# Optimization experiments

Measured on AMD Instinct MI355X. Metric: run time of the kernel, lower is better.

The kernel has to match this reference:

```python
import jax, jax.numpy as jnp
import numpy as np

NUM, B, C, H, W = 2, 8, 512, 32, 32


def setup_inputs() -> dict:
    key = jax.random.key(0)
    ks = jax.random.split(key, 6)
    s = 0.02  # weight init scale
    return {
        "feat_sources": jax.random.normal(ks[0], (NUM, B, C, H, W), jnp.float32),
        "feat_targets": jax.random.normal(ks[1], (NUM, B, C, H, W), jnp.float32),
        # 1x1 conv == per-pixel channel matmul: weight [num, C_out, C_in], bias [num, C]
        "Wq": jax.random.normal(ks[2], (NUM, C, C), jnp.float32) * s,
        "bq": jnp.zeros((NUM, C), jnp.float32),
        "Wk": jax.random.normal(ks[3], (NUM, C, C), jnp.float32) * s,
        "bk": jnp.zeros((NUM, C), jnp.float32),
        "Wv": jax.random.normal(ks[4], (NUM, C, C), jnp.float32) * s,
        "bv": jnp.zeros((NUM, C), jnp.float32),
    }


def reference(feat_sources, feat_targets, Wq, bq, Wk, bk, Wv, bv):
    num, Bt, Ct, Ht, Wt = feat_targets.shape
    HW = Ht * Wt
    tgt = feat_targets.reshape(num, Bt, Ct, HW)  # queries/values come from targets
    src = feat_sources.reshape(num, Bt, Ct, HW)  # keys come from sources

    # 1x1 conv projections (batched over the `num` heads of convs)
    Q = jnp.einsum('ioc,ibcn->ibno', Wq, tgt) + bq[:, None, None, :]   # (num, B, HW, C)
    K = jnp.einsum('joc,jbcn->jbon', Wk, src) + bk[:, None, :, None]   # (num, B, C, HW)
    V = jnp.einsum('ioc,ibcn->ibon', Wv, tgt) + bv[:, None, :, None]   # (num, B, C, HW)

    # energy[i, j] = bmm(pro_query_i, pro_key_j) over all target/source pairs
    energy = jnp.einsum('ibnc,jbcm->ijbnm', Q, K)                      # (num, num, B, HW, HW)

    # alpha: softmax over sources j of the scalar mean energy per (i, j)
    means = energy.mean(axis=(2, 3, 4))                                # (num, num)
    alphas = jax.nn.softmax(means, axis=1)

    # per-source softmax over keys, then summed across sources (torch.stack(...).sum(0))
    attn = jax.nn.softmax(energy, axis=-1).sum(axis=1)                 # (num, B, HW, HW)

    # out[b, c, n] = sum_m V[b, c, m] * attn[b, n, m]  (bmm(value, attention^T))
    out = jnp.einsum('ibcm,ibnm->ibcn', V, attn).reshape(num, Bt, Ct, Ht, Wt)
    return out, alphas
```

## Files before the change

kernel.cpp:

```cpp
#include <hip/hip_runtime.h>

#define NUMH 2
#define BATCH 8
#define CCH 512
#define HWN 1024

typedef unsigned short u16;
typedef unsigned int u32;
typedef _Float16 f16;
typedef __attribute__((ext_vector_type(8))) _Float16 f16x8;
typedef __attribute__((ext_vector_type(8))) short bf16x8;
typedef __attribute__((ext_vector_type(4))) float f32x4;

__device__ __forceinline__ u16 f2h(float x) {
    union { f16 h; u16 u; } cv;
    cv.h = (f16)x;
    return cv.u;
}
__device__ __forceinline__ u16 f2bf(float x) {
    u32 u = __float_as_uint(x);
    return (u16)((u + 0x7fffu + ((u >> 16) & 1u)) >> 16);
}

__device__ __forceinline__ float waveReduceSum(float v) {
#pragma unroll
    for (int off = 32; off > 0; off >>= 1) v += __shfl_xor(v, off);
    return v;
}

__device__ __forceinline__ void swz_decode(int& x, int& y, int& z) {
    const int gx = gridDim.x, gy = gridDim.y;
    const int nwg = gx * gy * gridDim.z;
    const int fid = blockIdx.x + gx * (blockIdx.y + gy * blockIdx.z);
    const int cpx = nwg >> 3;
    int swz = (fid & 7) * cpx + (fid >> 3);
    x = swz % gx; swz /= gx;
    y = swz % gy; z = swz / gy;
}

__global__ void zero_means_kernel(float* means) {
    if (threadIdx.x < 4) means[threadIdx.x] = 0.0f;
}
__global__ void zero_rs_kernel(float* rs, int n) {
    const int i = blockIdx.x * 256 + threadIdx.x;
    if (i < n) rs[i] = 0.0f;
}

__device__ __forceinline__ void stage_tile(const u16* __restrict__ src, int ld, int k0,
                                           u16* lds_arr, int w, int l) {
#pragma unroll
    for (int inst = 0; inst < 2; inst++) {
        const int p = w * 128 + inst * 64 + l;
        const int n = p >> 2;
        const int k4 = (p & 3) ^ ((n >> 1) & 3);
        const u16* g = src + n * ld + k0 + k4 * 8;
        u16* lp = lds_arr + (w * 128 + inst * 64) * 8;
        __builtin_amdgcn_global_load_lds(
            (const __attribute__((address_space(1))) u32*)g,
            (__attribute__((address_space(3))) u32*)lp, 16, 0, 0);
    }
}

template<bool BF>
__device__ __forceinline__ void mfma_block(const u16* sA, const u16* sB,
                                           int wr, int wc, int fr, int kq, f32x4 acc[4][4]) {
#define SLOT(row) (((row) * 4 + ((kq) ^ (((row) >> 1) & 3))) * 8)
    if constexpr (BF) {
        bf16x8 a[4], b[4];
#pragma unroll
        for (int mi = 0; mi < 4; mi++) a[mi] = *(const bf16x8*)(sA + SLOT(wr * 64 + mi * 16 + fr));
#pragma unroll
        for (int ni = 0; ni < 4; ni++) b[ni] = *(const bf16x8*)(sB + SLOT(wc * 64 + ni * 16 + fr));
#pragma unroll
        for (int mi = 0; mi < 4; mi++)
#pragma unroll
            for (int ni = 0; ni < 4; ni++)
                acc[mi][ni] = __builtin_amdgcn_mfma_f32_16x16x32_bf16(a[mi], b[ni], acc[mi][ni], 0, 0, 0);
    } else {
        f16x8 a[4], b[4];
#pragma unroll
        for (int mi = 0; mi < 4; mi++) a[mi] = *(const f16x8*)(sA + SLOT(wr * 64 + mi * 16 + fr));
#pragma unroll
        for (int ni = 0; ni < 4; ni++) b[ni] = *(const f16x8*)(sB + SLOT(wc * 64 + ni * 16 + fr));
#pragma unroll
        for (int mi = 0; mi < 4; mi++)
#pragma unroll
            for (int ni = 0; ni < 4; ni++)
                acc[mi][ni] = __builtin_amdgcn_mfma_f32_16x16x32_f16(a[mi], b[ni], acc[mi][ni], 0, 0, 0);
    }
#undef SLOT
}

template<bool BF>
__device__ __forceinline__ void mm_core(const u16* __restrict__ A, const u16* __restrict__ B,
                                        int K, int ldA, int ldB, u16* s, f32x4 acc[4][4]) {
    const int t = threadIdx.x, w = t >> 6, l = t & 63;
    const int wr = w >> 1, wc = w & 1, fr = l & 15, kq = l >> 4;
    u16 *sA0 = s, *sA1 = s + 4096, *sB0 = s + 8192, *sB1 = s + 12288;
    for (int k0 = 0; k0 < K; k0 += 64) {
        __syncthreads();
        stage_tile(A, ldA, k0, sA0, w, l);
        stage_tile(A, ldA, k0 + 32, sA1, w, l);
        stage_tile(B, ldB, k0, sB0, w, l);
        stage_tile(B, ldB, k0 + 32, sB1, w, l);
        __syncthreads();
        mfma_block<BF>(sA0, sB0, wr, wc, fr, kq, acc);
        mfma_block<BF>(sA1, sB1, wr, wc, fr, kq, acc);
    }
}

#define ACC_INIT(acc)                                         \
    f32x4 acc[4][4];                                          \
    _Pragma("unroll") for (int mi_ = 0; mi_ < 4; mi_++)       \
    _Pragma("unroll") for (int ni_ = 0; ni_ < 4; ni_++)       \
        acc[mi_][ni_] = (f32x4){0.f, 0.f, 0.f, 0.f};

#define SMEM_BYTES 32768

template<bool BF, bool BCOL, bool BROW>
__device__ __forceinline__ void epi_h16(char* smem, const f32x4 acc[4][4],
                                        const float* biasCol, const float* biasRow,
                                        u16* O, int ldO) {
    const int t = threadIdx.x, w = t >> 6, l = t & 63;
    const int wr = w >> 1, wc = w & 1, fr = l & 15, fq = l >> 4;
    u16* sb16 = (u16*)smem;
    u32* sb32 = (u32*)smem;
#pragma unroll
    for (int half = 0; half < 2; half++) {
        __syncthreads();
        if (wr == half) {
#pragma unroll
            for (int ni = 0; ni < 4; ni++) {
                const int col = wc * 64 + ni * 16 + fr;
                const float bc = BCOL ? biasCol[col] : 0.0f;
#pragma unroll
                for (int mi = 0; mi < 4; mi++)
#pragma unroll
                    for (int r = 0; r < 4; r++) {
                        const int lrow = mi * 16 + fq * 4 + r;
                        const float v = acc[mi][ni][r] + bc +
                                        (BROW ? biasRow[half * 64 + lrow] : 0.0f);
                        sb16[lrow * 132 + col] = BF ? f2bf(v) : f2h(v);
                    }
            }
        }
        __syncthreads();
#pragma unroll
        for (int it = 0; it < 4; it++) {
            const int idx = it * 256 + t;
            const int rr = idx >> 4, ch = idx & 15;
            const uint4 v4 = *(const uint4*)&sb32[rr * 66 + ch * 4];
            *(uint4*)&O[(size_t)(half * 64 + rr) * ldO + ch * 8] = v4;
        }
    }
}

template<bool SCALE>
__device__ __forceinline__ void epi_f32(char* smem, const f32x4 acc[4][4],
                                        const float* ls, float* O, int ldO) {
    const int t = threadIdx.x, w = t >> 6, l = t & 63;
    const int wr = w >> 1, wc = w & 1, fr = l & 15, fq = l >> 4;
    float* sf = (float*)smem;
#pragma unroll
    for (int q = 0; q < 4; q++) {
        __syncthreads();
        if (wr == (q >> 1)) {
            const int mi0 = (q & 1) * 2;
#pragma unroll
            for (int ni = 0; ni < 4; ni++) {
                const int col = wc * 64 + ni * 16 + fr;
                const float inv = SCALE ? 1.0f / ls[col] : 1.0f;
#pragma unroll
                for (int mm = 0; mm < 2; mm++)
#pragma unroll
                    for (int r = 0; r < 4; r++) {
                        const int lrow = mm * 16 + fq * 4 + r;
                        sf[lrow * 132 + col] = acc[mi0 + mm][ni][r] * inv;
                    }
            }
        }
        __syncthreads();
#pragma unroll
        for (int it = 0; it < 4; it++) {
            const int idx = it * 256 + t;
            const int rr = idx >> 5, ch = idx & 31;
            const float4 v4 = *(const float4*)&sf[rr * 132 + ch * 4];
            *(float4*)&O[(size_t)(q * 32 + rr) * ldO + ch * 4] = v4;
        }
    }
}

__global__ __launch_bounds__(256) void tconv_kernel(
    const float* __restrict__ tgt, const float* __restrict__ src,
    u16* __restrict__ Tt, u16* __restrict__ St) {
    __shared__ float s[64][65];
    const int z = blockIdx.z;
    const int ib = z & 15;
    const float* X = (z >> 4 ? src : tgt) + (size_t)ib * CCH * HWN;
    u16* O = (z >> 4 ? St : Tt) + (size_t)ib * HWN * CCH;
    const int n0 = blockIdx.x * 64, c0 = blockIdx.y * 64;
    const int t = threadIdx.x;
    {
        const int cc = t >> 4, nch = (t & 15) * 4;
#pragma unroll
        for (int r = 0; r < 4; r++) {
            const float4 v = *(const float4*)&X[(size_t)(c0 + cc + r * 16) * HWN + n0 + nch];
            s[cc + r * 16][nch + 0] = v.x;
            s[cc + r * 16][nch + 1] = v.y;
            s[cc + r * 16][nch + 2] = v.z;
            s[cc + r * 16][nch + 3] = v.w;
        }
    }
    __syncthreads();
    const int nl = t >> 2;
    const int cb = (t & 3) * 16;
    __attribute__((aligned(16))) u16 hbuf[16];
#pragma unroll
    for (int cc = 0; cc < 16; cc++) hbuf[cc] = f2h(s[cb + cc][nl]);
    const size_t orow = (size_t)(n0 + nl) * CCH + c0 + cb;
    *(uint4*)&O[orow + 0] = *(const uint4*)&hbuf[0];
    *(uint4*)&O[orow + 8] = *(const uint4*)&hbuf[8];
}

__global__ __launch_bounds__(256) void convw_kernel(
    const float* __restrict__ Wq, const float* __restrict__ Wk, const float* __restrict__ Wv,
    u16* __restrict__ Wqh, u16* __restrict__ Wkh, u16* __restrict__ Wvh) {
    const int idx = (blockIdx.x * 256 + threadIdx.x) * 4;
    {
        const float4 v = *(const float4*)&Wq[idx];
        uint2 h = {(u32)f2h(v.x) | ((u32)f2h(v.y) << 16), (u32)f2h(v.z) | ((u32)f2h(v.w) << 16)};
        *(uint2*)&Wqh[idx] = h;
    }
    {
        const float4 v = *(const float4*)&Wk[idx];
        uint2 h = {(u32)f2h(v.x) | ((u32)f2h(v.y) << 16), (u32)f2h(v.z) | ((u32)f2h(v.w) << 16)};
        *(uint2*)&Wkh[idx] = h;
    }
    {
        const float4 v = *(const float4*)&Wv[idx];
        uint2 h = {(u32)f2h(v.x) | ((u32)f2h(v.y) << 16), (u32)f2h(v.z) | ((u32)f2h(v.w) << 16)};
        *(uint2*)&Wvh[idx] = h;
    }
}

__global__ __launch_bounds__(256) void proj_qk_kernel(
    const u16* __restrict__ Tt, const u16* __restrict__ St,
    const u16* __restrict__ Wqh, const u16* __restrict__ Wkh,
    const float* __restrict__ bq, const float* __restrict__ bk,
    u16* __restrict__ Qp, u16* __restrict__ Kp) {
    __shared__ __align__(16) char smem[SMEM_BYTES];
    int bx, by, z;
    swz_decode(bx, by, z);
    const int b = z & 7, i = (z >> 3) & 1, p = z >> 4;
    const size_t ib = (size_t)(i * BATCH + b) * HWN * CCH;
    const u16* A = (p ? St : Tt) + ib;
    const u16* B = (p ? Wkh : Wqh) + (size_t)i * CCH * CCH;
    const float* bias = (p ? bk : bq) + i * CCH;
    u16* O = (p ? Kp : Qp) + ib;
    const int tile_m = by * 128, tile_n = bx * 128;

    ACC_INIT(acc)
    mm_core<false>(A + (size_t)tile_m * CCH, B + (size_t)tile_n * CCH,
                   CCH, CCH, CCH, (u16*)smem, acc);

    epi_h16<false, true, false>(smem, acc, bias + tile_n, nullptr,
                                O + (size_t)tile_m * CCH + tile_n, CCH);
}

__global__ __launch_bounds__(256) void proj_v_kernel(
    const u16* __restrict__ Wvh, const u16* __restrict__ Tt,
    const float* __restrict__ bvv, u16* __restrict__ Vb) {
    __shared__ __align__(16) char smem[SMEM_BYTES];
    int bx, by, z;
    swz_decode(bx, by, z);
    const int b = z & 7, i = z >> 3;
    const size_t ib = (size_t)(i * BATCH + b) * HWN * CCH;
    const u16* A = Wvh + (size_t)i * CCH * CCH;
    const u16* B = Tt + ib;
    const int tile_m = by * 128, tile_n = bx * 128;

    ACC_INIT(acc)
    mm_core<false>(A + (size_t)tile_m * CCH, B + (size_t)tile_n * CCH,
                   CCH, CCH, CCH, (u16*)smem, acc);

    u16* Ov = Vb + (size_t)(i * BATCH + b) * CCH * HWN;
    epi_h16<true, false, true>(smem, acc, nullptr, bvv + i * CCH + tile_m,
                               Ov + (size_t)tile_m * HWN + tile_n, HWN);
}

__global__ __launch_bounds__(256) void gemmE_kernel(
    const u16* __restrict__ Qp, const u16* __restrict__ Kp,
    u16* __restrict__ P, float* __restrict__ rs, float* __restrict__ means,
    int b0, int Bc) {
    __shared__ __align__(16) char smem[SMEM_BYTES];
    int bx, by, z;
    swz_decode(bx, by, z);
    const int j = z & 1, ib2 = z >> 1;
    const int i = ib2 / Bc, bb = ib2 % Bc, b = b0 + bb;
    const size_t offA = (size_t)(i * BATCH + b) * HWN * CCH;
    const size_t offB = (size_t)(j * BATCH + b) * HWN * CCH;
    const int tile_m = by * 128, tile_n = bx * 128;
    u16* Po = P + (size_t)(ib2 * 2 + j) * HWN * HWN + (size_t)tile_m * HWN + tile_n;
    float* rsp = rs + (size_t)(ib2 * 2 + j) * HWN;

    ACC_INIT(acc)
    mm_core<false>(Qp + offA + (size_t)tile_m * CCH, Kp + offB + (size_t)tile_n * CCH,
                   CCH, CCH, CCH, (u16*)smem, acc);

    const int t = threadIdx.x, w = t >> 6, l = t & 63;
    const int wr = w >> 1, wc = w & 1, fr = l & 15, fq = l >> 4;
    u16* sb16 = (u16*)smem;
    u32* sb32 = (u32*)smem;
    float* redsum = (float*)(smem + 17408);
    float tsum = 0.0f;
    float rowacc[4][4];
#pragma unroll
    for (int mi = 0; mi < 4; mi++)
#pragma unroll
        for (int r = 0; r < 4; r++) rowacc[mi][r] = 0.0f;
#pragma unroll
    for (int half = 0; half < 2; half++) {
        __syncthreads();
        if (wr == half) {
#pragma unroll
            for (int ni = 0; ni < 4; ni++) {
                const int col = wc * 64 + ni * 16 + fr;
#pragma unroll
                for (int mi = 0; mi < 4; mi++)
#pragma unroll
                    for (int r = 0; r < 4; r++) {
                        const int lrow = mi * 16 + fq * 4 + r;
                        const float raw = acc[mi][ni][r];
                        tsum += raw;
                        const float ex = __expf(raw);
                        rowacc[mi][r] += ex;
                        sb16[lrow * 132 + col] = f2bf(ex);
                    }
            }
        }
        __syncthreads();
#pragma unroll
        for (int it = 0; it < 4; it++) {
            const int idx = it * 256 + t;
            const int rr = idx >> 4, ch = idx & 15;
            const uint4 v4 = *(const uint4*)&sb32[rr * 66 + ch * 4];
            *(uint4*)&Po[(size_t)(half * 64 + rr) * HWN + ch * 8] = v4;
        }
    }
    tsum = waveReduceSum(tsum);
    if (l == 0) redsum[w] = tsum;
#pragma unroll
    for (int mi = 0; mi < 4; mi++)
#pragma unroll
        for (int r = 0; r < 4; r++) {
            float v = rowacc[mi][r];
            v += __shfl_xor(v, 1); v += __shfl_xor(v, 2);
            v += __shfl_xor(v, 4); v += __shfl_xor(v, 8);
            if (fr == 0) atomicAdd(&rsp[tile_m + wr * 64 + mi * 16 + fq * 4 + r], v);
        }
    __syncthreads();
    if (t == 0) atomicAdd(&means[i * 2 + j], redsum[0] + redsum[1] + redsum[2] + redsum[3]);
}

__global__ __launch_bounds__(256) void gemmOut_kernel(
    const u16* __restrict__ Vb, const u16* __restrict__ P, const float* __restrict__ rs,
    float* __restrict__ outp, int b0, int Bc) {
    __shared__ __align__(16) char smem[SMEM_BYTES];
    int bx, by, ib2;
    swz_decode(bx, by, ib2);
    const int i = ib2 / Bc, bb = ib2 % Bc, b = b0 + bb;
    const u16* A = Vb + (size_t)(i * BATCH + b) * CCH * HWN;
    const u16* P0 = P + (size_t)(ib2 * 2 + 0) * HWN * HWN;
    const u16* P1 = P + (size_t)(ib2 * 2 + 1) * HWN * HWN;
    const float* rs0 = rs + (size_t)(ib2 * 2 + 0) * HWN;
    const float* rs1 = rs + (size_t)(ib2 * 2 + 1) * HWN;
    float* O = outp + (size_t)(i * BATCH + b) * CCH * HWN;
    const int tile_m = by * 128, tile_n = bx * 128;
    const int t = threadIdx.x, w = t >> 6, l = t & 63;
    const int wc = w & 1, fr = l & 15;

    ACC_INIT(acc)
    mm_core<true>(A + (size_t)tile_m * HWN, P0 + (size_t)tile_n * HWN,
                  HWN, HWN, HWN, (u16*)smem, acc);
#pragma unroll
    for (int ni = 0; ni < 4; ni++) {
        const int col = tile_n + wc * 64 + ni * 16 + fr;
        const float sc = rs1[col] / rs0[col];
#pragma unroll
        for (int mi = 0; mi < 4; mi++) acc[mi][ni] *= sc;
    }
    mm_core<true>(A + (size_t)tile_m * HWN, P1 + (size_t)tile_n * HWN,
                  HWN, HWN, HWN, (u16*)smem, acc);

    epi_f32<true>(smem, acc, rs1 + tile_n, O + (size_t)tile_m * HWN + tile_n, HWN);
}

__global__ void alphas_kernel(const float* __restrict__ means, float* __restrict__ outp) {
    if (threadIdx.x != 0) return;
    const float cnt = (float)BATCH * (float)HWN * (float)HWN;
    float m[4];
#pragma unroll
    for (int k = 0; k < 4; k++) m[k] = means[k] / cnt;
#pragma unroll
    for (int i = 0; i < 2; i++) {
        const float a = m[i * 2 + 0], bsc = m[i * 2 + 1];
        const float mx = fmaxf(a, bsc);
        const float ea = __expf(a - mx), eb = __expf(bsc - mx);
        const float inv = 1.0f / (ea + eb);
        outp[i * 2 + 0] = ea * inv;
        outp[i * 2 + 1] = eb * inv;
    }
}

extern "C" void kernel_launch(void* const* d_in, const int* in_sizes, int n_in,
                              void* d_out, int out_size, void* d_ws, size_t ws_size,
                              hipStream_t stream) {
    const float* fsrc = (const float*)d_in[0];
    const float* ftgt = (const float*)d_in[1];
    const float* Wq = (const float*)d_in[2];
    const float* bq = (const float*)d_in[3];
    const float* Wk = (const float*)d_in[4];
    const float* bk = (const float*)d_in[5];
    const float* Wv = (const float*)d_in[6];
    const float* bv = (const float*)d_in[7];
    float* outp = (float*)d_out;

    const size_t SZ_ACT = (size_t)NUMH * BATCH * HWN * CCH * 2;
    const size_t SZ_W = (size_t)NUMH * CCH * CCH * 2;
    char* w = (char*)d_ws;
    u16* Qp = (u16*)w; w += SZ_ACT;
    u16* Kp = (u16*)w; w += SZ_ACT;
    u16* Vb = (u16*)w; w += SZ_ACT;
    u16* Wqh = (u16*)w; w += SZ_W;
    u16* Wkh = (u16*)w; w += SZ_W;
    u16* Wvh = (u16*)w; w += SZ_W;
    float* means = (float*)w; w += 64;
    float* rs = (float*)w; w += (size_t)NUMH * BATCH * 2 * HWN * 4;
    char* region = w;
    u16* Tt = (u16*)region;
    u16* St = (u16*)(region + SZ_ACT);

    const size_t base_used = (size_t)(region - (char*)d_ws);
    int Bc = 8;
    while (Bc > 1) {
        size_t need = (size_t)NUMH * Bc * 2 * HWN * HWN * 2;
        size_t tneed = need > 2 * SZ_ACT ? need : 2 * SZ_ACT;
        if (base_used + tneed <= ws_size) break;
        Bc >>= 1;
    }
    u16* P = (u16*)region;
    const int nrs = NUMH * Bc * 2 * HWN;

    zero_means_kernel<<<1, 64, 0, stream>>>(means);
    convw_kernel<<<512, 256, 0, stream>>>(Wq, Wk, Wv, Wqh, Wkh, Wvh);
    tconv_kernel<<<dim3(16, 8, 32), 256, 0, stream>>>(ftgt, fsrc, Tt, St);
    proj_qk_kernel<<<dim3(4, 8, 32), 256, 0, stream>>>(Tt, St, Wqh, Wkh, bq, bk, Qp, Kp);
    proj_v_kernel<<<dim3(8, 4, 16), 256, 0, stream>>>(Wvh, Tt, bv, Vb);

    const int nch = BATCH / Bc;
    for (int ch = 0; ch < nch; ch++) {
        const int b0 = ch * Bc;
        zero_rs_kernel<<<(nrs + 255) / 256, 256, 0, stream>>>(rs, nrs);
        gemmE_kernel<<<dim3(8, 8, NUMH * Bc * 2), 256, 0, stream>>>(Qp, Kp, P, rs, means, b0, Bc);
        gemmOut_kernel<<<dim3(8, 4, NUMH * Bc), 256, 0, stream>>>(Vb, P, rs, outp, b0, Bc);
    }
    alphas_kernel<<<1, 1, 0, stream>>>(means, outp + (out_size - 4));
}
```

Baseline: 211.2 us.

## Replace row-sum atomics with per-slice partial buffers and single-pass epilogue

Row sums of exp(energy) are no longer accumulated with global atomics into a zeroed buffer. Each column-slice (bx, wc) of gemmE writes its partial sums to its own slot, and gemmOut adds up the 16 partials per column itself, which removes the zero_rs kernel launch. The gemmE epilogue now stages the whole 128x128 bf16 tile in LDS at once instead of two halves, cutting barriers, and redsum moves to its own shared array. In exchange the rs buffer grows 16x, gemmOut does extra reads at its start, and gemmE uses a larger LDS footprint, which may lower occupancy.

```diff
diff --git a/kernel.cpp b/kernel.cpp
--- a/kernel.cpp
+++ b/kernel.cpp
@@ -40,10 +40,6 @@
 
 __global__ void zero_means_kernel(float* means) {
     if (threadIdx.x < 4) means[threadIdx.x] = 0.0f;
-}
-__global__ void zero_rs_kernel(float* rs, int n) {
-    const int i = blockIdx.x * 256 + threadIdx.x;
-    if (i < n) rs[i] = 0.0f;
 }
 
 __device__ __forceinline__ void stage_tile(const u16* __restrict__ src, int ld, int k0,
@@ -157,7 +153,7 @@
 
 template<bool SCALE>
 __device__ __forceinline__ void epi_f32(char* smem, const f32x4 acc[4][4],
-                                        const float* ls, float* O, int ldO) {
+                                        const float* inv4, float* O, int ldO) {
     const int t = threadIdx.x, w = t >> 6, l = t & 63;
     const int wr = w >> 1, wc = w & 1, fr = l & 15, fq = l >> 4;
     float* sf = (float*)smem;
@@ -169,7 +165,7 @@
 #pragma unroll
             for (int ni = 0; ni < 4; ni++) {
                 const int col = wc * 64 + ni * 16 + fr;
-                const float inv = SCALE ? 1.0f / ls[col] : 1.0f;
+                const float inv = SCALE ? inv4[ni] : 1.0f;
 #pragma unroll
                 for (int mm = 0; mm < 2; mm++)
 #pragma unroll
@@ -292,7 +288,8 @@
     const u16* __restrict__ Qp, const u16* __restrict__ Kp,
     u16* __restrict__ P, float* __restrict__ rs, float* __restrict__ means,
     int b0, int Bc) {
-    __shared__ __align__(16) char smem[SMEM_BYTES];
+    __shared__ __align__(16) char smem[33792];
+    __shared__ float redsum[4];
     int bx, by, z;
     swz_decode(bx, by, z);
     const int j = z & 1, ib2 = z >> 1;
@@ -301,7 +298,6 @@
     const size_t offB = (size_t)(j * BATCH + b) * HWN * CCH;
     const int tile_m = by * 128, tile_n = bx * 128;
     u16* Po = P + (size_t)(ib2 * 2 + j) * HWN * HWN + (size_t)tile_m * HWN + tile_n;
-    float* rsp = rs + (size_t)(ib2 * 2 + j) * HWN;
 
     ACC_INIT(acc)
     mm_core<false>(Qp + offA + (size_t)tile_m * CCH, Kp + offB + (size_t)tile_n * CCH,
@@ -311,7 +307,8 @@
     const int wr = w >> 1, wc = w & 1, fr = l & 15, fq = l >> 4;
     u16* sb16 = (u16*)smem;
     u32* sb32 = (u32*)smem;
-    float* redsum = (float*)(smem + 17408);
+    float* rsp = rs + ((size_t)(ib2 * 2 + j) * 16 + (bx * 2 + wc)) * HWN;
+    __syncthreads();
     float tsum = 0.0f;
     float rowacc[4][4];
 #pragma unroll
@@ -319,33 +316,19 @@
 #pragma unroll
         for (int r = 0; r < 4; r++) rowacc[mi][r] = 0.0f;
 #pragma unroll
-    for (int half = 0; half < 2; half++) {
-        __syncthreads();
-        if (wr == half) {
-#pragma unroll
-            for (int ni = 0; ni < 4; ni++) {
-                const int col = wc * 64 + ni * 16 + fr;
-#pragma unroll
-                for (int mi = 0; mi < 4; mi++)
-#pragma unroll
-                    for (int r = 0; r < 4; r++) {
-                        const int lrow = mi * 16 + fq * 4 + r;
-                        const float raw = acc[mi][ni][r];
-                        tsum += raw;
-                        const float ex = __expf(raw);
-                        rowacc[mi][r] += ex;
-                        sb16[lrow * 132 + col] = f2bf(ex);
-                    }
+    for (int ni = 0; ni < 4; ni++) {
+        const int col = wc * 64 + ni * 16 + fr;
+#pragma unroll
+        for (int mi = 0; mi < 4; mi++)
+#pragma unroll
+            for (int r = 0; r < 4; r++) {
+                const int row = wr * 64 + mi * 16 + fq * 4 + r;
+                const float raw = acc[mi][ni][r];
+                tsum += raw;
+                const float ex = __expf(raw);
+                rowacc[mi][r] += ex;
+                sb16[row * 132 + col] = f2bf(ex);
             }
-        }
-        __syncthreads();
-#pragma unroll
-        for (int it = 0; it < 4; it++) {
-            const int idx = it * 256 + t;
-            const int rr = idx >> 4, ch = idx & 15;
-            const uint4 v4 = *(const uint4*)&sb32[rr * 66 + ch * 4];
-            *(uint4*)&Po[(size_t)(half * 64 + rr) * HWN + ch * 8] = v4;
-        }
     }
     tsum = waveReduceSum(tsum);
     if (l == 0) redsum[w] = tsum;
@@ -356,10 +339,17 @@
             float v = rowacc[mi][r];
             v += __shfl_xor(v, 1); v += __shfl_xor(v, 2);
             v += __shfl_xor(v, 4); v += __shfl_xor(v, 8);
-            if (fr == 0) atomicAdd(&rsp[tile_m + wr * 64 + mi * 16 + fq * 4 + r], v);
+            if (fr == 0) rsp[tile_m + wr * 64 + mi * 16 + fq * 4 + r] = v;
         }
     __syncthreads();
     if (t == 0) atomicAdd(&means[i * 2 + j], redsum[0] + redsum[1] + redsum[2] + redsum[3]);
+#pragma unroll
+    for (int it = 0; it < 8; it++) {
+        const int idx = it * 256 + t;
+        const int rr = idx >> 4, ch = idx & 15;
+        const uint4 v4 = *(const uint4*)&sb32[rr * 66 + ch * 4];
+        *(uint4*)&Po[(size_t)rr * HWN + ch * 8] = v4;
+    }
 }
 
 __global__ __launch_bounds__(256) void gemmOut_kernel(
@@ -372,27 +362,38 @@
     const u16* A = Vb + (size_t)(i * BATCH + b) * CCH * HWN;
     const u16* P0 = P + (size_t)(ib2 * 2 + 0) * HWN * HWN;
     const u16* P1 = P + (size_t)(ib2 * 2 + 1) * HWN * HWN;
-    const float* rs0 = rs + (size_t)(ib2 * 2 + 0) * HWN;
-    const float* rs1 = rs + (size_t)(ib2 * 2 + 1) * HWN;
+    const float* rs0p = rs + (size_t)(ib2 * 2 + 0) * 16 * HWN;
+    const float* rs1p = rs + (size_t)(ib2 * 2 + 1) * 16 * HWN;
     float* O = outp + (size_t)(i * BATCH + b) * CCH * HWN;
     const int tile_m = by * 128, tile_n = bx * 128;
     const int t = threadIdx.x, w = t >> 6, l = t & 63;
     const int wc = w & 1, fr = l & 15;
 
+    float sc[4], inv4[4];
+#pragma unroll
+    for (int ni = 0; ni < 4; ni++) {
+        const int col = tile_n + wc * 64 + ni * 16 + fr;
+        float s0 = 0.0f, s1 = 0.0f;
+#pragma unroll
+        for (int sl = 0; sl < 16; sl++) {
+            s0 += rs0p[sl * HWN + col];
+            s1 += rs1p[sl * HWN + col];
+        }
+        sc[ni] = s1 / s0;
+        inv4[ni] = 1.0f / s1;
+    }
+
     ACC_INIT(acc)
     mm_core<true>(A + (size_t)tile_m * HWN, P0 + (size_t)tile_n * HWN,
                   HWN, HWN, HWN, (u16*)smem, acc);
 #pragma unroll
-    for (int ni = 0; ni < 4; ni++) {
-        const int col = tile_n + wc * 64 + ni * 16 + fr;
-        const float sc = rs1[col] / rs0[col];
-#pragma unroll
-        for (int mi = 0; mi < 4; mi++) acc[mi][ni] *= sc;
-    }
+    for (int ni = 0; ni < 4; ni++)
+#pragma unroll
+        for (int mi = 0; mi < 4; mi++) acc[mi][ni] *= sc[ni];
     mm_core<true>(A + (size_t)tile_m * HWN, P1 + (size_t)tile_n * HWN,
                   HWN, HWN, HWN, (u16*)smem, acc);
 
-    epi_f32<true>(smem, acc, rs1 + tile_n, O + (size_t)tile_m * HWN + tile_n, HWN);
+    epi_f32<true>(smem, acc, inv4, O + (size_t)tile_m * HWN + tile_n, HWN);
 }
 
 __global__ void alphas_kernel(const float* __restrict__ means, float* __restrict__ outp) {
@@ -435,7 +436,7 @@
     u16* Wkh = (u16*)w; w += SZ_W;
     u16* Wvh = (u16*)w; w += SZ_W;
     float* means = (float*)w; w += 64;
-    float* rs = (float*)w; w += (size_t)NUMH * BATCH * 2 * HWN * 4;
+    float* rs = (float*)w; w += (size_t)NUMH * BATCH * 2 * 16 * HWN * 4;
     char* region = w;
     u16* Tt = (u16*)region;
     u16* St = (u16*)(region + SZ_ACT);
@@ -449,7 +450,6 @@
         Bc >>= 1;
     }
     u16* P = (u16*)region;
-    const int nrs = NUMH * Bc * 2 * HWN;
 
     zero_means_kernel<<<1, 64, 0, stream>>>(means);
     convw_kernel<<<512, 256, 0, stream>>>(Wq, Wk, Wv, Wqh, Wkh, Wvh);
@@ -460,7 +460,6 @@
     const int nch = BATCH / Bc;
     for (int ch = 0; ch < nch; ch++) {
         const int b0 = ch * Bc;
-        zero_rs_kernel<<<(nrs + 255) / 256, 256, 0, stream>>>(rs, nrs);
         gemmE_kernel<<<dim3(8, 8, NUMH * Bc * 2), 256, 0, stream>>>(Qp, Kp, P, rs, means, b0, Bc);
         gemmOut_kernel<<<dim3(8, 4, NUMH * Bc), 256, 0, stream>>>(Vb, P, rs, outp, b0, Bc);
     }
```

Result: slower. 219.3 us (+3.8%).
